# Optimization experiments

Hardware: AMD Instinct MI355X
Metric: run time of the kernel (lower is better)

Reference implementation:

```python
import jax, jax.numpy as jnp
import numpy as np

V, D, H = 50000, 256, 4
HD = H * D            # concat head dim (TransformerConv concat=True)
HH, O = 256, 256      # invariant_hidden_dim, invariant_out_dim
B, N, E, L, A = 16, 1000, 4000, 64, 128
PAD = 0
SCALE = 1.0 / float(np.sqrt(D))


def emb_lookup(table, idx):
    # nn.Embedding with padding_idx: forward is a plain gather; grad at pad row is zeroed.
    rows = table[idx]
    return jnp.where((idx == PAD)[..., None], jax.lax.stop_gradient(rows), rows)


def transformer_conv(x, edge_index, ea, Wq, bq, Wk, bk, Wv, bv, We, Wskip, bskip):
    # PyG TransformerConv, heads=H, concat=True, root_weight=True, beta=False, dropout=0 (eval)
    n = x.shape[0]
    src, dst = edge_index[0], edge_index[1]
    q = (x @ Wq + bq).reshape(n, H, D)
    e = (ea @ We).reshape(-1, H, D)          # lin_edge (bias=False)
    k = (x @ Wk + bk).reshape(n, H, D)[src] + e
    v = (x @ Wv + bv).reshape(n, H, D)[src] + e
    alpha = (q[dst] * k).sum(-1) * SCALE      # [E,H]
    amax = jax.ops.segment_max(alpha, dst, num_segments=n)
    ex = jnp.exp(alpha - amax[dst])
    denom = jax.ops.segment_sum(ex, dst, num_segments=n)
    w = ex / denom[dst]                       # per-target-node softmax over incoming edges
    agg = jax.ops.segment_sum(v * w[..., None], dst, num_segments=n)
    return agg.reshape(n, HD) + x @ Wskip + bskip  # lin_skip on root


def mixed_embed(tok, node, graph_repr, emb):
    fixed = emb_lookup(emb, tok)
    flex = jnp.take_along_axis(graph_repr, node[..., None], axis=1)
    flex = jnp.where((node == PAD)[..., None], jax.lax.stop_gradient(flex), flex)
    return fixed + flex


def gru_last(xs, W_ih, W_hh, b_ih, b_hh):
    # torch nn.GRU, batch_first, 1 layer; only last hidden state is used
    gx = jnp.einsum('blh,gh->blg', xs, W_ih) + b_ih  # [B,L,3O]

    def step(h, g):
        gh = h @ W_hh.T + b_hh
        xr, xz, xn = jnp.split(g, 3, axis=-1)
        hr, hz, hn = jnp.split(gh, 3, axis=-1)
        r = jax.nn.sigmoid(xr + hr)
        z = jax.nn.sigmoid(xz + hz)
        c = jnp.tanh(xn + r * hn)
        return (1.0 - z) * c + z * h, None

    h0 = jnp.zeros((xs.shape[0], W_hh.shape[1]), xs.dtype)
    h_last, _ = jax.lax.scan(step, h0, jnp.swapaxes(gx, 0, 1))
    return h_last


def setup_inputs() -> dict:
    key = jax.random.key(0)
    ks = jax.random.split(key, 40)
    f = lambda i, shape, s=0.05: jax.random.normal(ks[i], shape, jnp.float32) * s
    ri = lambda i, shape, hi: jax.random.randint(ks[i], shape, 0, hi)
    return {
        'node_tokens': ri(0, (B, N), V),
        'edge_tokens': ri(1, (B, E), V),
        'edge_index': ri(2, (B, 2, E), N),
        'inv_token': ri(3, (B, L), V),
        'inv_node': ri(4, (B, L), N),
        'aa_token': ri(5, (B, A), V),
        'aa_node': ri(6, (B, A), N),
        'action_mask': jnp.ones((B, A), jnp.float32),
        'emb': f(7, (V, D), 0.02),
        'Wq': f(8, (D, HD)), 'bq': f(9, (HD,)),
        'Wk': f(10, (D, HD)), 'bk': f(11, (HD,)),
        'Wv': f(12, (D, HD)), 'bv': f(13, (HD,)),
        'We': f(14, (D, HD)),
        'Wskip': f(15, (D, HD)), 'bskip': f(16, (HD,)),
        'W1': f(17, (HD, D)), 'b1': f(18, (D,)),
        'Wp': f(19, (D, HH)), 'bp': f(20, (HH,)),
        'W_ih': f(21, (3 * O, HH)), 'W_hh': f(22, (3 * O, O)),
        'b_ih': f(23, (3 * O,)), 'b_hh': f(24, (3 * O,)),
        'Wab': f(25, (D, 1)), 'bab': f(26, (1,)),
        'Wap': f(27, (D, O)), 'bap': f(28, (O,)),
    }


def reference(node_tokens, edge_tokens, edge_index, inv_token, inv_node, aa_token, aa_node,
              action_mask, emb, Wq, bq, Wk, bk, Wv, bv, We, Wskip, bskip, W1, b1,
              Wp, bp, W_ih, W_hh, b_ih, b_hh, Wab, bab, Wap, bap):
    x = emb_lookup(emb, node_tokens)    # [B,N,D]
    ea = emb_lookup(emb, edge_tokens)   # [B,E,D]
    conv = jax.vmap(lambda xx, ei, ee: transformer_conv(
        xx, ei, ee, Wq, bq, Wk, bk, Wv, bv, We, Wskip, bskip))
    h = jax.nn.relu(conv(x, edge_index, ea))            # [B,N,HD]
    graph_repr = jax.nn.relu(h @ W1 + b1)               # [B,N,D]
    inv_h = jax.nn.relu(mixed_embed(inv_token, inv_node, graph_repr, emb) @ Wp + bp)
    inv = gru_last(inv_h, W_ih, W_hh, b_ih, b_hh)       # [B,O]
    aa_emb = mixed_embed(aa_token, aa_node, graph_repr, emb)  # [B,A,D]
    scores = jnp.einsum('bao,bo->ba', aa_emb @ Wap + bap, inv) + (aa_emb @ Wab + bab)[..., 0]
    inf_mask = jnp.maximum(jnp.log(action_mask), jnp.float32(np.finfo(np.float32).min))
    return scores + inf_mask
```

## Files before the change

### kernel.cpp

```cpp
#include <hip/hip_runtime.h>
#include <hip/hip_bf16.h>
#include <float.h>
#include <math.h>

typedef __hip_bfloat16 bf16;

#define B_ 16
#define N_ 1000
#define E_ 4000
#define L_ 64
#define A_ 128
#define D_ 256
#define H_ 4
#define HD_ 1024
#define SCALE_ 0.0625f

typedef __attribute__((ext_vector_type(8))) short short8;
typedef __attribute__((ext_vector_type(4))) float f32x4;

union U4S8 { uint4 u; short8 s; };

__device__ __forceinline__ unsigned short f2bf(float f) {
    bf16 h = __float2bfloat16(f);
    return *reinterpret_cast<unsigned short*>(&h);
}
__device__ __forceinline__ unsigned pack2(float a, float b) {
    return (unsigned)f2bf(a) | ((unsigned)f2bf(b) << 16);
}
__device__ __forceinline__ unsigned short rne1(float a) {
    unsigned ua = __float_as_uint(a);
    ua += 0x7fff + ((ua >> 16) & 1);
    return (unsigned short)(ua >> 16);
}
__device__ __forceinline__ float bflo(unsigned u) { return __uint_as_float(u << 16); }
__device__ __forceinline__ float bfhi(unsigned u) { return __uint_as_float(u & 0xffff0000u); }

#define LOG2E 1.4426950408889634f
__device__ __forceinline__ float fsigm(float x) {
    return __builtin_amdgcn_rcpf(1.f + __builtin_amdgcn_exp2f(-LOG2E * x));
}
__device__ __forceinline__ float ftanh(float x) {
    return 1.f - 2.f * __builtin_amdgcn_rcpf(1.f + __builtin_amdgcn_exp2f(2.f * LOG2E * x));
}

__global__ void convemb_kernel(const float* __restrict__ src, bf16* __restrict__ dst, long n4)
{
    long i = (long)blockIdx.x * 256 + threadIdx.x;
    if (i >= n4) return;
    float4 v = *(const float4*)(src + i * 4);
    *(uint2*)(dst + i * 4) = make_uint2(pack2(v.x, v.y), pack2(v.z, v.w));
}

__global__ void pack_all_kernel(const float* __restrict__ Wq, const float* __restrict__ Wk,
                                const float* __restrict__ Wv, const float* __restrict__ Wskip,
                                const float* __restrict__ We, const float* __restrict__ W1,
                                const float* __restrict__ Wp, const float* __restrict__ W_ih,
                                const float* __restrict__ Wap, const float* __restrict__ W_hh,
                                const float* __restrict__ bq, const float* __restrict__ bk,
                                const float* __restrict__ bv, const float* __restrict__ bskip,
                                unsigned* __restrict__ qkvsP, unsigned* __restrict__ WeP,
                                unsigned* __restrict__ W1P, unsigned* __restrict__ WpP,
                                unsigned* __restrict__ WihP, unsigned* __restrict__ WapP,
                                short8* __restrict__ WhhP, float* __restrict__ bias4096)
{
    int i = blockIdx.x * 256 + threadIdx.x;
    if (i < 524288) {
        int k2 = i >> 12, n = i & 4095;
        const float* s = (n < 1024) ? Wq : (n < 2048) ? Wk : (n < 3072) ? Wv : Wskip;
        int col = n & 1023;
        qkvsP[i] = pack2(s[(long)(2 * k2) * 1024 + col], s[(long)(2 * k2 + 1) * 1024 + col]);
        return;
    }
    i -= 524288;
    if (i < 131072) {
        int k2 = i >> 10, n = i & 1023;
        WeP[i] = pack2(We[(long)(2 * k2) * 1024 + n], We[(long)(2 * k2 + 1) * 1024 + n]);
        return;
    }
    i -= 131072;
    if (i < 131072) {
        int k2 = i >> 8, n = i & 255;
        W1P[i] = pack2(W1[(long)(2 * k2) * 256 + n], W1[(long)(2 * k2 + 1) * 256 + n]);
        return;
    }
    i -= 131072;
    if (i < 32768) {
        int k2 = i >> 8, n = i & 255;
        WpP[i] = pack2(Wp[(long)(2 * k2) * 256 + n], Wp[(long)(2 * k2 + 1) * 256 + n]);
        return;
    }
    i -= 32768;
    if (i < 98304) {
        int k2 = i / 768, n = i % 768;
        WihP[i] = pack2(W_ih[(long)n * 256 + 2 * k2], W_ih[(long)n * 256 + 2 * k2 + 1]);
        return;
    }
    i -= 98304;
    if (i < 32768) {
        int k2 = i >> 8, n = i & 255;
        WapP[i] = pack2(Wap[(long)(2 * k2) * 256 + n], Wap[(long)(2 * k2 + 1) * 256 + n]);
        return;
    }
    i -= 32768;
    if (i < 24576) {
        int lane = i & 63, tk = (i >> 6) & 7, tile = i >> 9;
        int n = tile * 16 + (lane & 15);
        const float* wp = W_hh + (long)n * 256 + tk * 32 + (lane >> 4) * 8;
        float4 w0 = *(const float4*)wp;
        float4 w1 = *(const float4*)(wp + 4);
        U4S8 u;
        u.u = make_uint4(pack2(w0.x, w0.y), pack2(w0.z, w0.w),
                         pack2(w1.x, w1.y), pack2(w1.z, w1.w));
        WhhP[i] = u.s;
        return;
    }
    i -= 24576;
    if (i < 4096) {
        int q = i >> 10, c = i & 1023;
        bias4096[i] = ((q == 0) ? bq : (q == 1) ? bk : (q == 2) ? bv : bskip)[c];
    }
}
#define PACK_ALL_TOT (524288 + 131072 + 131072 + 32768 + 98304 + 32768 + 24576 + 4096)

__global__ void gxt_kernel(const bf16* __restrict__ gxh, bf16* __restrict__ gxT)
{
    int i = blockIdx.x * 256 + threadIdx.x;
    if (i >= B_ * L_ * 768) return;
    int b = i / (L_ * 768);
    int rem = i - b * (L_ * 768);
    int t = rem / 768, n = rem - (rem / 768) * 768;
    gxT[((long)t * 768 + n) * 16 + b] = gxh[i];
}

#define TM 128
#define TN 128
#define TK 32
#define ASTR 40
#define BSTR 132

template <typename CT>
__global__ __launch_bounds__(256)
void pgemm_kernel(const bf16* __restrict__ A, const int* __restrict__ arows,
                  const unsigned* __restrict__ Bp, const float* __restrict__ bias,
                  CT* __restrict__ C, int M, int K, int Nc, int relu_out)
{
    __shared__ short    As[TM * ASTR];
    __shared__ unsigned Bs[(TK / 2) * BSTR];

    const int tid  = threadIdx.x;
    const int lane = tid & 63;
    const int wave = tid >> 6;
    const int wm = wave >> 1, wn = wave & 1;
    const int quad = lane >> 4, c16 = lane & 15;
    const long row0 = (long)blockIdx.y * TM;
    const int  col0 = blockIdx.x * TN;

    const int sm  = tid >> 1;
    const int sh  = (tid & 1) * 16;
    const int sn2 = tid & 63;
    const int skk = (tid >> 6) * 4;

    long gr_row = row0 + sm;
    if (gr_row > M - 1) gr_row = M - 1;
    long ar = arows ? (long)arows[gr_row] : gr_row;
    const short* Arow = (const short*)A + ar * K + sh;

    f32x4 acc[4][4];
    #pragma unroll
    for (int i = 0; i < 4; ++i)
        #pragma unroll
        for (int j = 0; j < 4; ++j)
            acc[i][j] = (f32x4){0.f, 0.f, 0.f, 0.f};

    for (int k0 = 0; k0 < K; k0 += TK) {
        {
            const short* p = Arow + k0;
            uint4 a = *(const uint4*)(p);
            uint4 b = *(const uint4*)(p + 8);
            *(uint4*)&As[sm * ASTR + sh]     = a;
            *(uint4*)&As[sm * ASTR + sh + 8] = b;
        }
        #pragma unroll
        for (int i = 0; i < 4; ++i) {
            int kk2 = skk + i;
            *(uint2*)&Bs[kk2 * BSTR + sn2 * 2] =
                *(const uint2*)&Bp[(long)(k0 / 2 + kk2) * Nc + col0 + sn2 * 2];
        }
        __syncthreads();

        short8 af[4];
        U4S8   bfr[4];
        #pragma unroll
        for (int mi = 0; mi < 4; ++mi) {
            int m = wm * 64 + mi * 16 + c16;
            af[mi] = *(const short8*)&As[m * ASTR + quad * 8];
        }
        #pragma unroll
        for (int ni = 0; ni < 4; ++ni) {
            int n = wn * 64 + ni * 16 + c16;
            uint4 u;
            u.x = Bs[(quad * 4 + 0) * BSTR + n];
            u.y = Bs[(quad * 4 + 1) * BSTR + n];
            u.z = Bs[(quad * 4 + 2) * BSTR + n];
            u.w = Bs[(quad * 4 + 3) * BSTR + n];
            bfr[ni].u = u;
        }
        #pragma unroll
        for (int mi = 0; mi < 4; ++mi)
            #pragma unroll
            for (int ni = 0; ni < 4; ++ni)
                acc[mi][ni] = __builtin_amdgcn_mfma_f32_16x16x32_bf16(
                    af[mi], bfr[ni].s, acc[mi][ni], 0, 0, 0);
        __syncthreads();
    }

    #pragma unroll
    for (int ni = 0; ni < 4; ++ni) {
        int col = col0 + wn * 64 + ni * 16 + c16;
        float bv = bias ? bias[col] : 0.f;
        #pragma unroll
        for (int mi = 0; mi < 4; ++mi) {
            long row = row0 + wm * 64 + mi * 16 + quad * 4;
            #pragma unroll
            for (int r = 0; r < 4; ++r) {
                if (row + r >= M) continue;
                float v = acc[mi][ni][r] + bv;
                if (relu_out) v = fmaxf(v, 0.f);
                C[(row + r) * Nc + col] = (CT)v;
            }
        }
    }
}

__global__ void zero_int_kernel(int* __restrict__ p, int n)
{
    int i = blockIdx.x * 256 + threadIdx.x;
    if (i < n) p[i] = 0;
}

__global__ void count_kernel(const int* __restrict__ edge_index, int b0,
                             int* __restrict__ cnt, int cE)
{
    int i = blockIdx.x * 256 + threadIdx.x;
    if (i >= cE) return;
    int bl = i / E_, ei = i % E_;
    int dst = edge_index[(long)(b0 + bl) * 2 * E_ + E_ + ei];
    atomicAdd(&cnt[bl * N_ + dst], 1);
}

__global__ __launch_bounds__(1024)
void scan_kernel(const int* __restrict__ cnt, int* __restrict__ row_start,
                 int* __restrict__ cursor)
{
    int bl = blockIdx.x;
    int tid = threadIdx.x;
    __shared__ int s[1024];
    int v = (tid < N_) ? cnt[bl * N_ + tid] : 0;
    s[tid] = v;
    __syncthreads();
    for (int off = 1; off < 1024; off <<= 1) {
        int t = (tid >= off) ? s[tid - off] : 0;
        __syncthreads();
        s[tid] += t;
        __syncthreads();
    }
    if (tid < N_) {
        int excl = s[tid] - v;
        row_start[bl * N_ + tid] = excl;
        cursor[bl * N_ + tid] = excl;
    }
}

__global__ void scatter_kernel(const int* __restrict__ edge_index, int b0,
                               int* __restrict__ cursor, int* __restrict__ elist, int cE)
{
    int i = blockIdx.x * 256 + threadIdx.x;
    if (i >= cE) return;
    int bl = i / E_, ei = i % E_;
    int dst = edge_index[(long)(b0 + bl) * 2 * E_ + E_ + ei];
    int pos = atomicAdd(&cursor[bl * N_ + dst], 1);
    elist[bl * E_ + pos] = ei;
}

__device__ __forceinline__ float qke2(unsigned q, unsigned k, unsigned e)
{
    return bflo(q) * (bflo(k) + bflo(e)) + bfhi(q) * (bfhi(k) + bfhi(e));
}

__global__ void alpha_ex_kernel(const bf16* __restrict__ qkvs, const bf16* __restrict__ e,
                                const int* __restrict__ edge_index,
                                int b0, float* __restrict__ ex, int cE)
{
    int eidx = blockIdx.x * 4 + (threadIdx.x >> 6);
    int l = threadIdx.x & 63;
    int bl = eidx / E_, ei = eidx % E_;
    const int* eb = edge_index + (long)(b0 + bl) * 2 * E_;
    int src = eb[ei], dst = eb[E_ + ei];
    int head = l >> 4;
    int j0 = head * 256 + (l & 15) * 16;

    const uint4* qp = (const uint4*)(qkvs + (long)(bl * N_ + dst) * 4096 + j0);
    const uint4* kp = (const uint4*)(qkvs + (long)(bl * N_ + src) * 4096 + 1024 + j0);
    const uint4* ep = (const uint4*)(e + (long)eidx * HD_ + j0);

    uint4 qa = qp[0], qb2 = qp[1];
    uint4 ka = kp[0], kb2 = kp[1];
    uint4 ea = ep[0], eb2 = ep[1];

    float s = qke2(qa.x, ka.x, ea.x) + qke2(qa.y, ka.y, ea.y)
            + qke2(qa.z, ka.z, ea.z) + qke2(qa.w, ka.w, ea.w)
            + qke2(qb2.x, kb2.x, eb2.x) + qke2(qb2.y, kb2.y, eb2.y)
            + qke2(qb2.z, kb2.z, eb2.z) + qke2(qb2.w, kb2.w, eb2.w);

    s += __shfl_down(s, 8);
    s += __shfl_down(s, 4);
    s += __shfl_down(s, 2);
    s += __shfl_down(s, 1);

    if ((l & 15) == 0)
        ex[(long)head * cE + eidx] = __builtin_amdgcn_exp2f(s * (SCALE_ * LOG2E));
}

__global__ void agg_node_kernel(const bf16* __restrict__ qkvs, const bf16* __restrict__ e,
                                const float* __restrict__ ex, const int* __restrict__ edge_index,
                                const int* __restrict__ row_start, const int* __restrict__ cnt,
                                const int* __restrict__ elist,
                                int b0, int cE, bf16* __restrict__ aggb)
{
    int base = blockIdx.x;
    int bl = base / N_;
    int tid = threadIdx.x;
    int h = tid >> 6;
    int j0 = tid * 4;

    int start = row_start[base];
    int deg = cnt[base];
    const int* el = elist + (long)bl * E_;
    const float* exh = ex + (long)h * cE;
    const int* srcp = edge_index + (long)(b0 + bl) * 2 * E_;

    float d = 0.f;
    for (int t = 0; t < deg; ++t)
        d += exh[(long)bl * E_ + el[start + t]];
    float invd = (deg > 0) ? 1.f / d : 0.f;

    float a0 = 0.f, a1 = 0.f, a2 = 0.f, a3 = 0.f;
    for (int t = 0; t < deg; ++t) {
        int ei = el[start + t];
        long eidx = (long)bl * E_ + ei;
        float w = exh[eidx] * invd;
        int src = srcp[ei];
        uint2 vv = *(const uint2*)(qkvs + (long)(bl * N_ + src) * 4096 + 2048 + j0);
        uint2 ee = *(const uint2*)(e + eidx * HD_ + j0);
        a0 += w * (bflo(vv.x) + bflo(ee.x));
        a1 += w * (bfhi(vv.x) + bfhi(ee.x));
        a2 += w * (bflo(vv.y) + bflo(ee.y));
        a3 += w * (bfhi(vv.y) + bfhi(ee.y));
    }

    uint2 sk = *(const uint2*)(qkvs + (long)base * 4096 + 3072 + j0);
    unsigned o0 = pack2(fmaxf(bflo(sk.x) + a0, 0.f), fmaxf(bfhi(sk.x) + a1, 0.f));
    unsigned o1 = pack2(fmaxf(bflo(sk.y) + a2, 0.f), fmaxf(bfhi(sk.y) + a3, 0.f));
    *(uint2*)(aggb + (long)base * HD_ + j0) = make_uint2(o0, o1);
}

__global__ void mixed2_kernel(const bf16* __restrict__ embh,
                              const int* __restrict__ inv_token, const int* __restrict__ inv_node,
                              const int* __restrict__ aa_token, const int* __restrict__ aa_node,
                              const float* __restrict__ graph_repr,
                              bf16* __restrict__ mixed_inv, bf16* __restrict__ aa_emb)
{
    int r = blockIdx.x;
    int d = threadIdx.x;
    if (r < B_ * L_) {
        int b = r / L_;
        float v = (float)embh[(long)inv_token[r] * D_ + d] +
                  graph_repr[((long)b * N_ + inv_node[r]) * D_ + d];
        mixed_inv[(long)r * D_ + d] = __float2bfloat16(v);
    } else {
        int r2 = r - B_ * L_;
        int b = r2 / A_;
        float v = (float)embh[(long)aa_token[r2] * D_ + d] +
                  graph_repr[((long)b * N_ + aa_node[r2]) * D_ + d];
        aa_emb[(long)r2 * D_ + d] = __float2bfloat16(v);
    }
}

__global__ __launch_bounds__(1024)
void gru_kernel(const bf16* __restrict__ gxT, const short8* __restrict__ WhhP,
                const float* __restrict__ b_hh, float* __restrict__ inv_out)
{
    __shared__ short hB[2][16 * 264];

    const int tid = threadIdx.x;
    const int lane = tid & 63;
    const int wave = tid >> 6;
    const int quad = lane >> 4, c16 = lane & 15;
    const int n0 = wave * 16 + c16;

    for (int i = tid; i < 2 * 16 * 264; i += 1024) ((short*)hB)[i] = 0;

    short8 wfr[8], wfz[8], wfn[8];
    #pragma unroll
    for (int tk = 0; tk < 8; ++tk) {
        wfr[tk] = WhhP[((0 * 16 + wave) * 8 + tk) * 64 + lane];
        wfz[tk] = WhhP[((1 * 16 + wave) * 8 + tk) * 64 + lane];
        wfn[tk] = WhhP[((2 * 16 + wave) * 8 + tk) * 64 + lane];
    }
    float bhr = b_hh[0 * 256 + n0];
    float bhz = b_hh[1 * 256 + n0];
    float bhn = b_hh[2 * 256 + n0];

    float myh0 = 0.f, myh1 = 0.f, myh2 = 0.f, myh3 = 0.f;

    const short* gbr = (const short*)gxT + (long)(0 * 256 + n0) * 16 + quad * 4;
    const short* gbz = gbr + 256 * 16;
    const short* gbn = gbr + 512 * 16;

    uint2 pxr = *(const uint2*)gbr;
    uint2 pxz = *(const uint2*)gbz;
    uint2 pxn = *(const uint2*)gbn;

    __syncthreads();

    int p = 0;
    for (int t = 0; t < L_; ++t) {
        uint2 xr2 = pxr, xz2 = pxz, xn2 = pxn;
        long noff = (long)((t + 1 < L_) ? t + 1 : t) * 12288;
        pxr = *(const uint2*)(gbr + noff);
        pxz = *(const uint2*)(gbz + noff);
        pxn = *(const uint2*)(gbn + noff);

        f32x4 ar = (f32x4){bhr, bhr, bhr, bhr};
        f32x4 az = (f32x4){bhz, bhz, bhz, bhz};
        f32x4 an = (f32x4){bhn, bhn, bhn, bhn};
        const short* hp = &hB[p][0];
        #pragma unroll
        for (int tk = 0; tk < 8; ++tk) {
            short8 a = *(const short8*)&hp[c16 * 264 + tk * 32 + quad * 8];
            ar = __builtin_amdgcn_mfma_f32_16x16x32_bf16(a, wfr[tk], ar, 0, 0, 0);
            az = __builtin_amdgcn_mfma_f32_16x16x32_bf16(a, wfz[tk], az, 0, 0, 0);
            an = __builtin_amdgcn_mfma_f32_16x16x32_bf16(a, wfn[tk], an, 0, 0, 0);
        }

        float xr[4] = {bflo(xr2.x), bfhi(xr2.x), bflo(xr2.y), bfhi(xr2.y)};
        float xz[4] = {bflo(xz2.x), bfhi(xz2.x), bflo(xz2.y), bfhi(xz2.y)};
        float xn[4] = {bflo(xn2.x), bfhi(xn2.x), bflo(xn2.y), bfhi(xn2.y)};
        float hold[4] = {myh0, myh1, myh2, myh3};
        float hn[4];
        short* hw = &hB[p ^ 1][0];
        #pragma unroll
        for (int r = 0; r < 4; ++r) {
            float rr = fsigm(xr[r] + ar[r]);
            float zz = fsigm(xz[r] + az[r]);
            float cc = ftanh(xn[r] + rr * an[r]);
            hn[r] = (1.f - zz) * cc + zz * hold[r];
            hw[(quad * 4 + r) * 264 + n0] = (short)rne1(hn[r]);
        }
        myh0 = hn[0]; myh1 = hn[1]; myh2 = hn[2]; myh3 = hn[3];
        p ^= 1;
        __syncthreads();
    }

    inv_out[(long)(quad * 4 + 0) * 256 + n0] = myh0;
    inv_out[(long)(quad * 4 + 1) * 256 + n0] = myh1;
    inv_out[(long)(quad * 4 + 2) * 256 + n0] = myh2;
    inv_out[(long)(quad * 4 + 3) * 256 + n0] = myh3;
}

__global__ void score_kernel(const float* __restrict__ aa_p, const bf16* __restrict__ aa_emb,
                             const float* __restrict__ inv, const float* __restrict__ Wab,
                             const float* __restrict__ bab, const float* __restrict__ mask,
                             float* __restrict__ out)
{
    int r = blockIdx.x * 4 + (threadIdx.x >> 6);
    int l = threadIdx.x & 63;
    int b = r / A_;
    float s = 0.f;
    for (int d = l; d < D_; d += 64)
        s += aa_p[(long)r * D_ + d] * inv[(long)b * D_ + d] +
             (float)aa_emb[(long)r * D_ + d] * Wab[d];
    #pragma unroll
    for (int off = 32; off; off >>= 1) s += __shfl_down(s, off);
    if (l == 0) {
        float lm = logf(mask[r]);
        const float MN = -3.4028234663852886e38f;
        if (!(lm >= MN)) lm = MN;
        out[r] = s + bab[0] + lm;
    }
}

static inline size_t align256(size_t x) { return (x + 255) & ~(size_t)255; }

template <typename CT>
static void launch_pgemm(const bf16* A, const int* arows, const unsigned* Bp,
                         const float* bias, CT* C, int M, int K, int Nc, int relu,
                         hipStream_t s)
{
    dim3 grid(Nc / TN, (M + TM - 1) / TM);
    pgemm_kernel<CT><<<grid, 256, 0, s>>>(A, arows, Bp, bias, C, M, K, Nc, relu);
}

extern "C" void kernel_launch(void* const* d_in, const int* in_sizes, int n_in,
                              void* d_out, int out_size, void* d_ws, size_t ws_size,
                              hipStream_t stream)
{
    const int* node_tokens = (const int*)d_in[0];
    const int* edge_tokens = (const int*)d_in[1];
    const int* edge_index  = (const int*)d_in[2];
    const int* inv_token   = (const int*)d_in[3];
    const int* inv_node    = (const int*)d_in[4];
    const int* aa_token    = (const int*)d_in[5];
    const int* aa_node     = (const int*)d_in[6];
    const float* action_mask = (const float*)d_in[7];
    const float* emb   = (const float*)d_in[8];
    const float* Wq    = (const float*)d_in[9];
    const float* bq    = (const float*)d_in[10];
    const float* Wk    = (const float*)d_in[11];
    const float* bk    = (const float*)d_in[12];
    const float* Wv    = (const float*)d_in[13];
    const float* bv    = (const float*)d_in[14];
    const float* We    = (const float*)d_in[15];
    const float* Wskip = (const float*)d_in[16];
    const float* bskip = (const float*)d_in[17];
    const float* W1    = (const float*)d_in[18];
    const float* b1    = (const float*)d_in[19];
    const float* Wp    = (const float*)d_in[20];
    const float* bp    = (const float*)d_in[21];
    const float* W_ih  = (const float*)d_in[22];
    const float* W_hh  = (const float*)d_in[23];
    const float* b_ih  = (const float*)d_in[24];
    const float* b_hh  = (const float*)d_in[25];
    const float* Wab   = (const float*)d_in[26];
    const float* bab   = (const float*)d_in[27];
    const float* Wap   = (const float*)d_in[28];
    const float* bap   = (const float*)d_in[29];
    (void)in_sizes; (void)n_in; (void)out_size;

    char* base = (char*)d_ws;
    size_t off = 0;
    auto alloc = [&](size_t bytes) -> char* {
        char* p = base + off;
        off = align256(off + bytes);
        return p;
    };

    const long VD = 50000L * 256;
    bf16*  embh       = (bf16*)alloc(VD * 2);
    float* graph_repr = (float*)alloc((size_t)B_ * N_ * D_ * 4);
    bf16*  mixed_inv  = (bf16*)alloc((size_t)B_ * L_ * D_ * 2);
    bf16*  inv_h      = (bf16*)alloc((size_t)B_ * L_ * D_ * 2);
    bf16*  gxh        = (bf16*)alloc((size_t)B_ * L_ * 768 * 2);
    bf16*  gxT        = (bf16*)alloc((size_t)B_ * L_ * 768 * 2);
    float* inv_out    = (float*)alloc((size_t)B_ * 256 * 4);
    bf16*  aa_emb     = (bf16*)alloc((size_t)B_ * A_ * D_ * 2);
    float* aa_p       = (float*)alloc((size_t)B_ * A_ * 256 * 4);
    unsigned* qkvsP   = (unsigned*)alloc((size_t)128 * 4096 * 4);
    unsigned* WeP     = (unsigned*)alloc((size_t)128 * 1024 * 4);
    unsigned* W1P     = (unsigned*)alloc((size_t)512 * 256 * 4);
    unsigned* WpP     = (unsigned*)alloc((size_t)128 * 256 * 4);
    unsigned* WihP    = (unsigned*)alloc((size_t)128 * 768 * 4);
    unsigned* WapP    = (unsigned*)alloc((size_t)128 * 256 * 4);
    short8* WhhP      = (short8*)alloc((size_t)24576 * 16);
    float* bias4096   = (float*)alloc(4096 * 4);
    size_t persist = off;

    int c = 16;
    while (c > 1) {
        size_t cN = (size_t)c * N_, cEs = (size_t)c * E_;
        size_t chunk = align256(cN * 4096 * 2)
                     + align256(cEs * HD_ * 2)
                     + align256(cN * HD_ * 2)
                     + align256(cEs * H_ * 4)
                     + 3 * align256(cN * 4)
                     + align256(cEs * 4);
        if (persist + chunk <= ws_size) break;
        c >>= 1;
    }
    int cN = c * N_, cE = c * E_;

    bf16*  qkvs  = (bf16*)alloc((size_t)cN * 4096 * 2);
    bf16*  ebuf  = (bf16*)alloc((size_t)cE * HD_ * 2);
    bf16*  aggb  = (bf16*)alloc((size_t)cN * HD_ * 2);
    float* ex    = (float*)alloc((size_t)cE * H_ * 4);
    int*   cnt   = (int*)alloc((size_t)cN * 4);
    int*   rstart= (int*)alloc((size_t)cN * 4);
    int*   cursor= (int*)alloc((size_t)cN * 4);
    int*   elist = (int*)alloc((size_t)cE * 4);

    convemb_kernel<<<(int)((VD / 4 + 255) / 256), 256, 0, stream>>>(emb, embh, VD / 4);
    pack_all_kernel<<<(PACK_ALL_TOT + 255) / 256, 256, 0, stream>>>(
        Wq, Wk, Wv, Wskip, We, W1, Wp, W_ih, Wap, W_hh, bq, bk, bv, bskip,
        qkvsP, WeP, W1P, WpP, WihP, WapP, WhhP, bias4096);

    for (int b0 = 0; b0 < B_; b0 += c) {
        zero_int_kernel<<<(cN + 255) / 256, 256, 0, stream>>>(cnt, cN);
        count_kernel<<<(cE + 255) / 256, 256, 0, stream>>>(edge_index, b0, cnt, cE);
        scan_kernel<<<c, 1024, 0, stream>>>(cnt, rstart, cursor);
        scatter_kernel<<<(cE + 255) / 256, 256, 0, stream>>>(edge_index, b0, cursor,
                                                             elist, cE);
        launch_pgemm<bf16>(embh, node_tokens + (long)b0 * N_, qkvsP, bias4096, qkvs,
                           cN, D_, 4096, 0, stream);
        launch_pgemm<bf16>(embh, edge_tokens + (long)b0 * E_, WeP, nullptr, ebuf,
                           cE, D_, HD_, 0, stream);
        alpha_ex_kernel<<<cE / 4, 256, 0, stream>>>(qkvs, ebuf, edge_index, b0, ex, cE);
        agg_node_kernel<<<cN, 256, 0, stream>>>(qkvs, ebuf, ex, edge_index, rstart, cnt,
                                                elist, b0, cE, aggb);
        launch_pgemm<float>(aggb, nullptr, W1P, b1,
                            graph_repr + (long)b0 * N_ * D_, cN, HD_, D_, 1, stream);
    }

    mixed2_kernel<<<B_ * L_ + B_ * A_, 256, 0, stream>>>(embh, inv_token, inv_node,
                                                         aa_token, aa_node, graph_repr,
                                                         mixed_inv, aa_emb);
    launch_pgemm<bf16>(mixed_inv, nullptr, WpP, bp, inv_h, B_ * L_, D_, 256, 1, stream);
    launch_pgemm<bf16>(inv_h, nullptr, WihP, b_ih, gxh, B_ * L_, 256, 768, 0, stream);
    gxt_kernel<<<(B_ * L_ * 768 + 255) / 256, 256, 0, stream>>>(gxh, gxT);
    gru_kernel<<<1, 1024, 0, stream>>>(gxT, WhhP, b_hh, inv_out);

    launch_pgemm<float>(aa_emb, nullptr, WapP, bap, aa_p, B_ * A_, D_, 256, 0, stream);
    score_kernel<<<(B_ * A_) / 4, 256, 0, stream>>>(aa_p, aa_emb, inv_out, Wab, bab,
                                                    action_mask, (float*)d_out);
}
```

Baseline: 888.4 us.

## Avoid materializing per-edge lin_edge projections via algebraic reassociation

The per-edge edge-embedding GEMM (E×256→1024) is no longer materialised. For attention, q·(ea We) is rewritten as (q We^T)·ea: a per-node GEMM against a transposed, per-head packed We produces qW, and the alpha kernel dots it with raw edge embeddings. For aggregation, softmax-weighted raw edge embeddings are summed per node and then projected through We in a GEMM that accumulates into the agg buffer, with the ReLU moved there. This swaps E-sized work for N-sized GEMMs and removes the large ebuf traffic, but adds extra launches and an extra bf16 rounding of intermediate sums.

```diff
diff --git a/kernel.cpp b/kernel.cpp
--- a/kernel.cpp
+++ b/kernel.cpp
@@ -61,6 +61,7 @@
                                 unsigned* __restrict__ qkvsP, unsigned* __restrict__ WeP,
                                 unsigned* __restrict__ W1P, unsigned* __restrict__ WpP,
                                 unsigned* __restrict__ WihP, unsigned* __restrict__ WapP,
+                                unsigned* __restrict__ WeTP,
                                 short8* __restrict__ WhhP, float* __restrict__ bias4096)
 {
     int i = blockIdx.x * 256 + threadIdx.x;
@@ -102,6 +103,14 @@
         return;
     }
     i -= 32768;
+    if (i < 131072) {
+        int k2 = i >> 10, n = i & 1023;
+        int d = n & 255, hb = n & ~255;
+        WeTP[i] = pack2(We[(long)d * 1024 + hb + 2 * k2],
+                        We[(long)d * 1024 + hb + 2 * k2 + 1]);
+        return;
+    }
+    i -= 131072;
     if (i < 24576) {
         int lane = i & 63, tk = (i >> 6) & 7, tile = i >> 9;
         int n = tile * 16 + (lane & 15);
@@ -120,7 +129,7 @@
         bias4096[i] = ((q == 0) ? bq : (q == 1) ? bk : (q == 2) ? bv : bskip)[c];
     }
 }
-#define PACK_ALL_TOT (524288 + 131072 + 131072 + 32768 + 98304 + 32768 + 24576 + 4096)
+#define PACK_ALL_TOT (524288 + 131072 + 131072 + 32768 + 98304 + 32768 + 131072 + 24576 + 4096)
 
 __global__ void gxt_kernel(const bf16* __restrict__ gxh, bf16* __restrict__ gxT)
 {
@@ -142,7 +151,8 @@
 __global__ __launch_bounds__(256)
 void pgemm_kernel(const bf16* __restrict__ A, const int* __restrict__ arows,
                   const unsigned* __restrict__ Bp, const float* __restrict__ bias,
-                  CT* __restrict__ C, int M, int K, int Nc, int relu_out)
+                  CT* __restrict__ C, int M, int K, int Nc, int relu_out,
+                  long astride, int aoff, int colbase, int hslice, int addC)
 {
     __shared__ short    As[TM * ASTR];
     __shared__ unsigned Bs[(TK / 2) * BSTR];
@@ -153,7 +163,8 @@
     const int wm = wave >> 1, wn = wave & 1;
     const int quad = lane >> 4, c16 = lane & 15;
     const long row0 = (long)blockIdx.y * TM;
-    const int  col0 = blockIdx.x * TN;
+    const int  col0 = colbase + blockIdx.x * TN;
+    const int  aoff2 = aoff + (hslice ? (col0 & ~255) : 0);
 
     const int sm  = tid >> 1;
     const int sh  = (tid & 1) * 16;
@@ -163,7 +174,7 @@
     long gr_row = row0 + sm;
     if (gr_row > M - 1) gr_row = M - 1;
     long ar = arows ? (long)arows[gr_row] : gr_row;
-    const short* Arow = (const short*)A + ar * K + sh;
+    const short* Arow = (const short*)A + ar * astride + aoff2 + sh;
 
     f32x4 acc[4][4];
     #pragma unroll
@@ -225,6 +236,7 @@
             for (int r = 0; r < 4; ++r) {
                 if (row + r >= M) continue;
                 float v = acc[mi][ni][r] + bv;
+                if (addC) v += (float)C[(row + r) * Nc + col];
                 if (relu_out) v = fmaxf(v, 0.f);
                 C[(row + r) * Nc + col] = (CT)v;
             }
@@ -282,12 +294,13 @@
     elist[bl * E_ + pos] = ei;
 }
 
-__device__ __forceinline__ float qke2(unsigned q, unsigned k, unsigned e)
-{
-    return bflo(q) * (bflo(k) + bflo(e)) + bfhi(q) * (bfhi(k) + bfhi(e));
-}
-
-__global__ void alpha_ex_kernel(const bf16* __restrict__ qkvs, const bf16* __restrict__ e,
+__device__ __forceinline__ float d2(unsigned a, unsigned b)
+{
+    return bflo(a) * bflo(b) + bfhi(a) * bfhi(b);
+}
+
+__global__ void alpha_ex_kernel(const bf16* __restrict__ qkvs, const bf16* __restrict__ qWb,
+                                const bf16* __restrict__ embh, const int* __restrict__ edge_tokens,
                                 const int* __restrict__ edge_index,
                                 int b0, float* __restrict__ ex, int cE)
 {
@@ -296,48 +309,56 @@
     int bl = eidx / E_, ei = eidx % E_;
     const int* eb = edge_index + (long)(b0 + bl) * 2 * E_;
     int src = eb[ei], dst = eb[E_ + ei];
+    int tok = edge_tokens[(long)(b0 + bl) * E_ + ei];
     int head = l >> 4;
-    int j0 = head * 256 + (l & 15) * 16;
-
-    const uint4* qp = (const uint4*)(qkvs + (long)(bl * N_ + dst) * 4096 + j0);
-    const uint4* kp = (const uint4*)(qkvs + (long)(bl * N_ + src) * 4096 + 1024 + j0);
-    const uint4* ep = (const uint4*)(e + (long)eidx * HD_ + j0);
+    int li = l & 15;
+    int joff = head * 256 + li * 16;
+
+    const uint4* qp = (const uint4*)(qkvs + (long)(bl * N_ + dst) * 4096 + joff);
+    const uint4* kp = (const uint4*)(qkvs + (long)(bl * N_ + src) * 4096 + 1024 + joff);
+    const uint4* wp = (const uint4*)(qWb + (long)(bl * N_ + dst) * 1024 + joff);
+    const uint4* xp = (const uint4*)(embh + (long)tok * 256 + li * 16);
 
     uint4 qa = qp[0], qb2 = qp[1];
     uint4 ka = kp[0], kb2 = kp[1];
-    uint4 ea = ep[0], eb2 = ep[1];
-
-    float s = qke2(qa.x, ka.x, ea.x) + qke2(qa.y, ka.y, ea.y)
-            + qke2(qa.z, ka.z, ea.z) + qke2(qa.w, ka.w, ea.w)
-            + qke2(qb2.x, kb2.x, eb2.x) + qke2(qb2.y, kb2.y, eb2.y)
-            + qke2(qb2.z, kb2.z, eb2.z) + qke2(qb2.w, kb2.w, eb2.w);
+    uint4 wa = wp[0], wb2 = wp[1];
+    uint4 xa = xp[0], xb2 = xp[1];
+
+    float s = d2(qa.x, ka.x) + d2(qa.y, ka.y) + d2(qa.z, ka.z) + d2(qa.w, ka.w)
+            + d2(qb2.x, kb2.x) + d2(qb2.y, kb2.y) + d2(qb2.z, kb2.z) + d2(qb2.w, kb2.w)
+            + d2(wa.x, xa.x) + d2(wa.y, xa.y) + d2(wa.z, xa.z) + d2(wa.w, xa.w)
+            + d2(wb2.x, xb2.x) + d2(wb2.y, xb2.y) + d2(wb2.z, xb2.z) + d2(wb2.w, xb2.w);
 
     s += __shfl_down(s, 8);
     s += __shfl_down(s, 4);
     s += __shfl_down(s, 2);
     s += __shfl_down(s, 1);
 
-    if ((l & 15) == 0)
+    if (li == 0)
         ex[(long)head * cE + eidx] = __builtin_amdgcn_exp2f(s * (SCALE_ * LOG2E));
 }
 
-__global__ void agg_node_kernel(const bf16* __restrict__ qkvs, const bf16* __restrict__ e,
+__global__ void agg_node_kernel(const bf16* __restrict__ qkvs, const bf16* __restrict__ embh,
+                                const int* __restrict__ edge_tokens,
                                 const float* __restrict__ ex, const int* __restrict__ edge_index,
                                 const int* __restrict__ row_start, const int* __restrict__ cnt,
                                 const int* __restrict__ elist,
-                                int b0, int cE, bf16* __restrict__ aggb)
+                                int b0, int cE, bf16* __restrict__ aggb,
+                                bf16* __restrict__ xsumb)
 {
     int base = blockIdx.x;
     int bl = base / N_;
     int tid = threadIdx.x;
     int h = tid >> 6;
     int j0 = tid * 4;
+    int jx = (tid & 63) * 4;
 
     int start = row_start[base];
     int deg = cnt[base];
     const int* el = elist + (long)bl * E_;
     const float* exh = ex + (long)h * cE;
     const int* srcp = edge_index + (long)(b0 + bl) * 2 * E_;
+    const int* tokp = edge_tokens + (long)(b0 + bl) * E_;
 
     float d = 0.f;
     for (int t = 0; t < deg; ++t)
@@ -345,23 +366,30 @@
     float invd = (deg > 0) ? 1.f / d : 0.f;
 
     float a0 = 0.f, a1 = 0.f, a2 = 0.f, a3 = 0.f;
+    float x0 = 0.f, x1 = 0.f, x2 = 0.f, x3 = 0.f;
     for (int t = 0; t < deg; ++t) {
         int ei = el[start + t];
         long eidx = (long)bl * E_ + ei;
         float w = exh[eidx] * invd;
         int src = srcp[ei];
+        int tok = tokp[ei];
         uint2 vv = *(const uint2*)(qkvs + (long)(bl * N_ + src) * 4096 + 2048 + j0);
-        uint2 ee = *(const uint2*)(e + eidx * HD_ + j0);
-        a0 += w * (bflo(vv.x) + bflo(ee.x));
-        a1 += w * (bfhi(vv.x) + bfhi(ee.x));
-        a2 += w * (bflo(vv.y) + bflo(ee.y));
-        a3 += w * (bfhi(vv.y) + bfhi(ee.y));
+        uint2 xx = *(const uint2*)(embh + (long)tok * 256 + jx);
+        a0 += w * bflo(vv.x);
+        a1 += w * bfhi(vv.x);
+        a2 += w * bflo(vv.y);
+        a3 += w * bfhi(vv.y);
+        x0 += w * bflo(xx.x);
+        x1 += w * bfhi(xx.x);
+        x2 += w * bflo(xx.y);
+        x3 += w * bfhi(xx.y);
     }
 
     uint2 sk = *(const uint2*)(qkvs + (long)base * 4096 + 3072 + j0);
-    unsigned o0 = pack2(fmaxf(bflo(sk.x) + a0, 0.f), fmaxf(bfhi(sk.x) + a1, 0.f));
-    unsigned o1 = pack2(fmaxf(bflo(sk.y) + a2, 0.f), fmaxf(bfhi(sk.y) + a3, 0.f));
+    unsigned o0 = pack2(bflo(sk.x) + a0, bfhi(sk.x) + a1);
+    unsigned o1 = pack2(bflo(sk.y) + a2, bfhi(sk.y) + a3);
     *(uint2*)(aggb + (long)base * HD_ + j0) = make_uint2(o0, o1);
+    *(uint2*)(xsumb + (long)base * HD_ + j0) = make_uint2(pack2(x0, x1), pack2(x2, x3));
 }
 
 __global__ void mixed2_kernel(const bf16* __restrict__ embh,
@@ -495,10 +523,12 @@
 template <typename CT>
 static void launch_pgemm(const bf16* A, const int* arows, const unsigned* Bp,
                          const float* bias, CT* C, int M, int K, int Nc, int relu,
-                         hipStream_t s)
-{
-    dim3 grid(Nc / TN, (M + TM - 1) / TM);
-    pgemm_kernel<CT><<<grid, 256, 0, s>>>(A, arows, Bp, bias, C, M, K, Nc, relu);
+                         long astride, int aoff, int colbase, int hslice, int addC,
+                         int ncols, hipStream_t s)
+{
+    dim3 grid(ncols / TN, (M + TM - 1) / TM);
+    pgemm_kernel<CT><<<grid, 256, 0, s>>>(A, arows, Bp, bias, C, M, K, Nc, relu,
+                                          astride, aoff, colbase, hslice, addC);
 }
 
 extern "C" void kernel_launch(void* const* d_in, const int* in_sizes, int n_in,
@@ -561,6 +591,7 @@
     unsigned* WpP     = (unsigned*)alloc((size_t)128 * 256 * 4);
     unsigned* WihP    = (unsigned*)alloc((size_t)128 * 768 * 4);
     unsigned* WapP    = (unsigned*)alloc((size_t)128 * 256 * 4);
+    unsigned* WeTP    = (unsigned*)alloc((size_t)128 * 1024 * 4);
     short8* WhhP      = (short8*)alloc((size_t)24576 * 16);
     float* bias4096   = (float*)alloc(4096 * 4);
     size_t persist = off;
@@ -569,7 +600,8 @@
     while (c > 1) {
         size_t cN = (size_t)c * N_, cEs = (size_t)c * E_;
         size_t chunk = align256(cN * 4096 * 2)
-                     + align256(cEs * HD_ * 2)
+                     + align256(cN * HD_ * 2)
+                     + align256(cN * HD_ * 2)
                      + align256(cN * HD_ * 2)
                      + align256(cEs * H_ * 4)
                      + 3 * align256(cN * 4)
@@ -580,8 +612,9 @@
     int cN = c * N_, cE = c * E_;
 
     bf16*  qkvs  = (bf16*)alloc((size_t)cN * 4096 * 2);
-    bf16*  ebuf  = (bf16*)alloc((size_t)cE * HD_ * 2);
+    bf16*  qWb   = (bf16*)alloc((size_t)cN * HD_ * 2);
     bf16*  aggb  = (bf16*)alloc((size_t)cN * HD_ * 2);
+    bf16*  xsumb = (bf16*)alloc((size_t)cN * HD_ * 2);
     float* ex    = (float*)alloc((size_t)cE * H_ * 4);
     int*   cnt   = (int*)alloc((size_t)cN * 4);
     int*   rstart= (int*)alloc((size_t)cN * 4);
@@ -591,7 +624,7 @@
     convemb_kernel<<<(int)((VD / 4 + 255) / 256), 256, 0, stream>>>(emb, embh, VD / 4);
     pack_all_kernel<<<(PACK_ALL_TOT + 255) / 256, 256, 0, stream>>>(
         Wq, Wk, Wv, Wskip, We, W1, Wp, W_ih, Wap, W_hh, bq, bk, bv, bskip,
-        qkvsP, WeP, W1P, WpP, WihP, WapP, WhhP, bias4096);
+        qkvsP, WeP, W1P, WpP, WihP, WapP, WeTP, WhhP, bias4096);
 
     for (int b0 = 0; b0 < B_; b0 += c) {
         zero_int_kernel<<<(cN + 255) / 256, 256, 0, stream>>>(cnt, cN);
@@ -600,25 +633,32 @@
         scatter_kernel<<<(cE + 255) / 256, 256, 0, stream>>>(edge_index, b0, cursor,
                                                              elist, cE);
         launch_pgemm<bf16>(embh, node_tokens + (long)b0 * N_, qkvsP, bias4096, qkvs,
-                           cN, D_, 4096, 0, stream);
-        launch_pgemm<bf16>(embh, edge_tokens + (long)b0 * E_, WeP, nullptr, ebuf,
-                           cE, D_, HD_, 0, stream);
-        alpha_ex_kernel<<<cE / 4, 256, 0, stream>>>(qkvs, ebuf, edge_index, b0, ex, cE);
-        agg_node_kernel<<<cN, 256, 0, stream>>>(qkvs, ebuf, ex, edge_index, rstart, cnt,
-                                                elist, b0, cE, aggb);
+                           cN, D_, 4096, 0, 256, 0, 0, 0, 0, 4096, stream);
+        launch_pgemm<bf16>(qkvs, nullptr, WeTP, nullptr, qWb,
+                           cN, 256, 1024, 0, 4096, 0, 0, 1, 0, 1024, stream);
+        alpha_ex_kernel<<<cE / 4, 256, 0, stream>>>(qkvs, qWb, embh, edge_tokens,
+                                                    edge_index, b0, ex, cE);
+        agg_node_kernel<<<cN, 256, 0, stream>>>(qkvs, embh, edge_tokens, ex, edge_index,
+                                                rstart, cnt, elist, b0, cE, aggb, xsumb);
+        launch_pgemm<bf16>(xsumb, nullptr, WeP, nullptr, aggb,
+                           cN, 256, 1024, 1, 1024, 0, 0, 1, 1, 1024, stream);
         launch_pgemm<float>(aggb, nullptr, W1P, b1,
-                            graph_repr + (long)b0 * N_ * D_, cN, HD_, D_, 1, stream);
+                            graph_repr + (long)b0 * N_ * D_,
+                            cN, HD_, D_, 1, 1024, 0, 0, 0, 0, 256, stream);
     }
 
     mixed2_kernel<<<B_ * L_ + B_ * A_, 256, 0, stream>>>(embh, inv_token, inv_node,
                                                          aa_token, aa_node, graph_repr,
                                                          mixed_inv, aa_emb);
-    launch_pgemm<bf16>(mixed_inv, nullptr, WpP, bp, inv_h, B_ * L_, D_, 256, 1, stream);
-    launch_pgemm<bf16>(inv_h, nullptr, WihP, b_ih, gxh, B_ * L_, 256, 768, 0, stream);
+    launch_pgemm<bf16>(mixed_inv, nullptr, WpP, bp, inv_h,
+                       B_ * L_, D_, 256, 1, 256, 0, 0, 0, 0, 256, stream);
+    launch_pgemm<bf16>(inv_h, nullptr, WihP, b_ih, gxh,
+                       B_ * L_, 256, 768, 0, 256, 0, 0, 0, 0, 768, stream);
     gxt_kernel<<<(B_ * L_ * 768 + 255) / 256, 256, 0, stream>>>(gxh, gxT);
     gru_kernel<<<1, 1024, 0, stream>>>(gxT, WhhP, b_hh, inv_out);
 
-    launch_pgemm<float>(aa_emb, nullptr, WapP, bap, aa_p, B_ * A_, D_, 256, 0, stream);
+    launch_pgemm<float>(aa_emb, nullptr, WapP, bap, aa_p,
+                        B_ * A_, D_, 256, 0, 256, 0, 0, 0, 0, 256, stream);
     score_kernel<<<(B_ * A_) / 4, 256, 0, stream>>>(aa_p, aa_emb, inv_out, Wab, bab,
                                                     action_mask, (float*)d_out);
 }
```

Result: no change. 880.3 us (-0.9%).
